# Optimization experiments

Hardware: AMD Instinct MI355X
Metric: run time of the kernel (lower is better)

Reference implementation:

```python
import jax, jax.numpy as jnp
import numpy as np
from jax import lax

_MS_SSIM_WEIGHTS = [0.0448, 0.2856, 0.3001, 0.2363, 0.1333]
LEVELS = 5
WINDOW_SIZE = 11
SIGMA = 1.5
DATA_RANGE = 2.0


def _gaussian_kernel(size, sigma, channels):
    x = jnp.arange(size, dtype=jnp.float32) - size // 2
    g = jnp.exp(-x ** 2 / (2.0 * sigma ** 2))
    g = g / g.sum()
    k2d = jnp.outer(g, g)  # [size, size]
    # depthwise kernel: [C, 1, size, size] (OIHW with feature_group_count=C)
    return jnp.broadcast_to(k2d[None, None], (channels, 1, size, size))


def _depthwise_conv(x, kernel, pad):
    C = x.shape[1]
    return lax.conv_general_dilated(
        x, kernel,
        window_strides=(1, 1),
        padding=[(pad, pad), (pad, pad)],
        dimension_numbers=('NCHW', 'OIHW', 'NCHW'),
        feature_group_count=C)


def _avg_pool2(x):
    s = lax.reduce_window(x, 0.0, lax.add, (1, 1, 2, 2), (1, 1, 2, 2), 'VALID')
    return s * 0.25


def _ssim(x, y, window_size=WINDOW_SIZE, sigma=SIGMA, data_range=DATA_RANGE):
    K1, K2 = 0.01, 0.03
    C1 = (K1 * data_range) ** 2
    C2 = (K2 * data_range) ** 2
    kernel = _gaussian_kernel(window_size, sigma, x.shape[1])
    pad = window_size // 2
    mu1 = _depthwise_conv(x, kernel, pad)
    mu2 = _depthwise_conv(y, kernel, pad)
    mu1_sq = mu1 * mu1
    mu2_sq = mu2 * mu2
    mu1_mu2 = mu1 * mu2
    sig1_sq = _depthwise_conv(x * x, kernel, pad) - mu1_sq
    sig2_sq = _depthwise_conv(y * y, kernel, pad) - mu2_sq
    sig12 = _depthwise_conv(x * y, kernel, pad) - mu1_mu2
    num = (2.0 * mu1_mu2 + C1) * (2.0 * sig12 + C2)
    den = (mu1_sq + mu2_sq + C1) * (sig1_sq + sig2_sq + C2)
    ssim_map = num / (den + 1e-8)
    return ssim_map.mean()


def setup_inputs() -> dict:
    key = jax.random.key(0)
    k1, k2 = jax.random.split(key)
    pred = jax.random.normal(k1, (16, 3, 512, 512), dtype=jnp.float32)
    target = jax.random.normal(k2, (16, 3, 512, 512), dtype=jnp.float32)
    return {"pred": pred, "target": target}


def reference(pred, target):
    weights = jnp.asarray(_MS_SSIM_WEIGHTS[:LEVELS], dtype=jnp.float32)
    weights = weights / weights.sum()
    ms_ssim_val = jnp.zeros((), dtype=jnp.float32)
    x, y = pred, target
    for i in range(LEVELS):
        s = _ssim(x, y)
        ms_ssim_val = ms_ssim_val + weights[i] * s
        if i < LEVELS - 1:
            x = _avg_pool2(x)
            y = _avg_pool2(y)
    return 1.0 - ms_ssim_val
```

## Files before the change

kernel.cpp:

```cpp
#include <hip/hip_runtime.h>


#define TW 32
#define NTHR 128
#define NIMG 48
#define WIN 42
#define PQ  32
#define NSLOT 256
#define SSTRIDE 16

#define RS1 272
#define RS2 144
#define RS3 80
#define RS4 48
#define IS0 (512L*512)
#define IS1 (256L*272)
#define IS2 (128L*144)
#define IS3 (64L*80)
#define IS4 (32L*48)

typedef float v4f __attribute__((ext_vector_type(4)));

struct Pyr {
    float *x1, *y1, *x2, *y2, *x3, *y3, *x4, *y4;
};

__device__ __forceinline__ void h_load(
    const float* __restrict__ xi, const float* __restrict__ yi,
    const float* __restrict__ zpad, int gr, int gc0, int H, int W,
    bool fastp, int rowStride, float* xv, float* yv)
{
    const bool rok = ((unsigned)gr < (unsigned)H);
    if (fastp) {
        const float* px = rok ? (xi + (long)gr * rowStride + gc0) : zpad;
        const float* py = rok ? (yi + (long)gr * rowStride + gc0) : zpad;
#pragma unroll
        for (int v = 0; v < 6; ++v) {
            const float4 a = reinterpret_cast<const float4*>(px)[v];
            const float4 b = reinterpret_cast<const float4*>(py)[v];
            xv[4*v+0]=a.x; xv[4*v+1]=a.y; xv[4*v+2]=a.z; xv[4*v+3]=a.w;
            yv[4*v+0]=b.x; yv[4*v+1]=b.y; yv[4*v+2]=b.z; yv[4*v+3]=b.w;
        }
    } else {
        const float* xrow = xi + (long)gr * rowStride;
        const float* yrow = yi + (long)gr * rowStride;
#pragma unroll
        for (int k = 3; k < 21; ++k) {
            const int gc = gc0 + k;
            const bool ok = rok && ((unsigned)gc < (unsigned)W);
            xv[k] = ok ? xrow[gc] : 0.0f;
            yv[k] = ok ? yrow[gc] : 0.0f;
        }
    }
}

__device__ __forceinline__ void h_conv_write(
    const float* xv, const float* yv, v4f* smA, int slot, int cb,
    const float* G)
{
    v4f s[8];
#pragma unroll
    for (int j = 0; j < 8; ++j) s[j] = {0.f, 0.f, 0.f, 0.f};
#pragma unroll
    for (int m = 0; m < 18; ++m) {
        const float a = xv[m+3], b = yv[m+3];
        v4f w; w.x = a; w.y = b; w.z = a*a + b*b; w.w = a*b;
#pragma unroll
        for (int j = 0; j < 8; ++j) {
            if (j <= m && m - j <= 10) {
                s[j] += w * G[m - j];
            }
        }
    }
    const int u = slot & 31;
#pragma unroll
    for (int j = 0; j < 8; ++j)
        smA[slot * PQ + ((cb + j) ^ u)] = s[j];
}

__device__ __forceinline__ float v_phase(
    const v4f* smA, int vb, int c, int rr0, int R0, int C0, int H, int W,
    const float* G)
{
    const float C1 = 4.0e-4f;
    const float C2 = 3.6e-3f;
    v4f acc[8];
#pragma unroll
    for (int i = 0; i < 8; ++i) acc[i] = {0.f, 0.f, 0.f, 0.f};
    int sl = vb;
#pragma unroll
    for (int k = 0; k < 18; ++k) {
        const v4f h = smA[sl * PQ + (c ^ (sl & 31))];
#pragma unroll
        for (int i = 0; i < 8; ++i) {
            if (i <= k && k - i <= 10) {
                acc[i] += h * G[k - i];
            }
        }
        sl = (sl + 1 == WIN) ? 0 : sl + 1;
    }
    float local = 0.f;
    const int gc = C0 + c;
#pragma unroll
    for (int i = 0; i < 8; ++i) {
        const int gr2 = R0 + rr0 + i;
        if (gr2 < H && gc < W) {
            const float mu1 = acc[i].x, mu2 = acc[i].y;
            const float mu1s = mu1*mu1, mu2s = mu2*mu2, m12 = mu1*mu2;
            const float ssum = acc[i].z - mu1s - mu2s;
            const float s12  = acc[i].w - m12;
            const float num = (2.f * m12 + C1) * (2.f * s12 + C2);
            const float den = (mu1s + mu2s + C1) * (ssum + C2);
            local += num * __builtin_amdgcn_rcpf(den + 1e-8f);
        }
    }
    return local;
}

__device__ __forceinline__ void pool_tree(
    const float* __restrict__ xi, const float* __restrict__ yi,
    int t, int R0, int C0, int z, const Pyr& p, int bx)
{
    const int r = t >> 3, c2 = t & 7;
    const int gr = R0 + 4 * r;
    const int gc = C0 + 4 * c2;

    float4 ax[4], ay[4];
#pragma unroll
    for (int rr = 0; rr < 4; ++rr) {
        ax[rr] = *reinterpret_cast<const float4*>(xi + (long)(gr+rr)*512 + gc);
        ay[rr] = *reinterpret_cast<const float4*>(yi + (long)(gr+rr)*512 + gc);
    }
    float qx[2][2], qy[2][2];
#pragma unroll
    for (int i = 0; i < 2; ++i) {
        qx[i][0] = 0.25f*(ax[2*i].x+ax[2*i].y+ax[2*i+1].x+ax[2*i+1].y);
        qx[i][1] = 0.25f*(ax[2*i].z+ax[2*i].w+ax[2*i+1].z+ax[2*i+1].w);
        qy[i][0] = 0.25f*(ay[2*i].x+ay[2*i].y+ay[2*i+1].x+ay[2*i+1].y);
        qy[i][1] = 0.25f*(ay[2*i].z+ay[2*i].w+ay[2*i+1].z+ay[2*i+1].w);
    }
    float* x1p = p.x1 + z*IS1;  float* y1p = p.y1 + z*IS1;
    float* x2p = p.x2 + z*IS2;  float* y2p = p.y2 + z*IS2;
    float* x3p = p.x3 + z*IS3;  float* y3p = p.y3 + z*IS3;
    float* x4p = p.x4 + z*IS4;  float* y4p = p.y4 + z*IS4;

    const int r1 = (R0 >> 1) + 2*r, c1 = (C0 >> 1) + 2*c2;
#pragma unroll
    for (int i = 0; i < 2; ++i) {
        *reinterpret_cast<float2*>(x1p + (long)(r1+i)*RS1 + c1) =
            make_float2(qx[i][0], qx[i][1]);
        *reinterpret_cast<float2*>(y1p + (long)(r1+i)*RS1 + c1) =
            make_float2(qy[i][0], qy[i][1]);
    }
    const float v2x = 0.25f*(qx[0][0]+qx[0][1]+qx[1][0]+qx[1][1]);
    const float v2y = 0.25f*(qy[0][0]+qy[0][1]+qy[1][0]+qy[1][1]);
    x2p[(long)((R0>>2)+r)*RS2 + (C0>>2)+c2] = v2x;
    y2p[(long)((R0>>2)+r)*RS2 + (C0>>2)+c2] = v2y;
    const float v3x = 0.25f*(v2x + __shfl_down(v2x,1,64)
                           + __shfl_down(v2x,8,64) + __shfl_down(v2x,9,64));
    const float v3y = 0.25f*(v2y + __shfl_down(v2y,1,64)
                           + __shfl_down(v2y,8,64) + __shfl_down(v2y,9,64));
    if (!(r & 1) && !(c2 & 1)) {
        x3p[(long)((R0>>3)+(r>>1))*RS3 + (C0>>3)+(c2>>1)] = v3x;
        y3p[(long)((R0>>3)+(r>>1))*RS3 + (C0>>3)+(c2>>1)] = v3y;
    }
    const float v4x = 0.25f*(v3x + __shfl_down(v3x,2,64)
                           + __shfl_down(v3x,16,64) + __shfl_down(v3x,18,64));
    const float v4y = 0.25f*(v3y + __shfl_down(v3y,2,64)
                           + __shfl_down(v3y,16,64) + __shfl_down(v3y,18,64));
    if (!(r & 3) && !(c2 & 3)) {
        x4p[(long)((R0>>4)+(r>>2))*RS4 + (C0>>4)+(c2>>2)] = v4x;
        y4p[(long)((R0>>4)+(r>>2))*RS4 + (C0>>4)+(c2>>2)] = v4y;
    }
    if (bx == 0) {
#pragma unroll
        for (int i = 0; i < 2; ++i) {
            x1p[(long)(r1+i)*RS1 + (c2-8)] = 0.f;
            y1p[(long)(r1+i)*RS1 + (c2-8)] = 0.f;
        }
        x2p[(long)((R0>>2)+r)*RS2 + (c2-8)] = 0.f;
        y2p[(long)((R0>>2)+r)*RS2 + (c2-8)] = 0.f;
        if (r < 4) { x3p[(long)((R0>>3)+r)*RS3 + (c2-8)] = 0.f;
                     y3p[(long)((R0>>3)+r)*RS3 + (c2-8)] = 0.f; }
        if (r < 2) { x4p[(long)((R0>>4)+r)*RS4 + (c2-8)] = 0.f;
                     y4p[(long)((R0>>4)+r)*RS4 + (c2-8)] = 0.f; }
    }
    if (bx == 15) {
#pragma unroll
        for (int i = 0; i < 2; ++i) {
            x1p[(long)(r1+i)*RS1 + 256 + c2] = 0.f;
            y1p[(long)(r1+i)*RS1 + 256 + c2] = 0.f;
        }
        x2p[(long)((R0>>2)+r)*RS2 + 128 + c2] = 0.f;
        y2p[(long)((R0>>2)+r)*RS2 + 128 + c2] = 0.f;
        if (r < 4) { x3p[(long)((R0>>3)+r)*RS3 + 64 + c2] = 0.f;
                     y3p[(long)((R0>>3)+r)*RS3 + 64 + c2] = 0.f; }
        if (r < 2) { x4p[(long)((R0>>4)+r)*RS4 + 32 + c2] = 0.f;
                     y4p[(long)((R0>>4)+r)*RS4 + 32 + c2] = 0.f; }
    }
}

__global__ __launch_bounds__(NTHR, 2) void ssim_l0_kernel(
    const float* __restrict__ x, const float* __restrict__ y,
    Pyr p, const float* __restrict__ zpad, float* __restrict__ slots)
{
    const float G[11] = {
        0.00102839f, 0.00759877f, 0.03600077f, 0.10936069f, 0.21300539f,
        0.26601173f, 0.21300539f, 0.10936069f, 0.03600077f, 0.00759877f,
        0.00102839f};

    __shared__ __align__(16) v4f smA[WIN * PQ];

    const int t    = threadIdx.x;
    const int bid  = blockIdx.x;
    const int tile = (bid & 7) * 384 + (bid >> 3);
    const int bx   = tile & 15;
    const int by   = (tile >> 4) & 3;
    const int z    = tile >> 6;
    const int C0   = bx * TW;
    const int S0   = by * 128;
    const float* xi = x + (long)z * IS0;
    const float* yi = y + (long)z * IS0;
    const bool fastp = (C0 >= 8) && (C0 + TW + 8 <= 512);

    for (int s = t; s < WIN * 4; s += NTHR) {
        const int r = s % WIN, q = s / WIN;
        float pxv[24], pyv[24];
        h_load(xi, yi, zpad, S0 + r - 5, C0 + (q << 3) - 8, 512, 512, fastp,
               512, pxv, pyv);
        h_conv_write(pxv, pyv, smA, r, q << 3, G);
    }
    __syncthreads();

    const int c    = t & 31;
    const int rr0  = (t >> 5) * 8;
    const int hr   = t & 31, hq = t >> 5;
    const int hgc0 = C0 + (hq << 3) - 8;
    int wslot = hr, vb = rr0;
    float local = 0.f;

    for (int tt = 0; tt < 3; ++tt) {
        const int R0 = S0 + 32 * tt;
        float xv[24], yv[24];
        h_load(xi, yi, zpad, R0 + 37 + hr, hgc0, 512, 512, fastp, 512, xv, yv);
        local += v_phase(smA, vb, c, rr0, R0, C0, 512, 512, G);
        if (t < 64) pool_tree(xi, yi, t, R0, C0, z, p, bx);
        __syncthreads();
        h_conv_write(xv, yv, smA, wslot, hq << 3, G);
        __syncthreads();
        wslot += 32; if (wslot >= WIN) wslot -= WIN;
        vb    += 32; if (vb    >= WIN) vb    -= WIN;
    }
    {
        const int R0 = S0 + 96;
        local += v_phase(smA, vb, c, rr0, R0, C0, 512, 512, G);
        if (t < 64) pool_tree(xi, yi, t, R0, C0, z, p, bx);
    }

#pragma unroll
    for (int off = 32; off > 0; off >>= 1) local += __shfl_down(local, off, 64);
    if ((t & 63) == 0) {
        const int slot = ((tile << 1) | (t >> 6)) & (NSLOT - 1);
        atomicAdd(slots + slot * SSTRIDE, local);
    }
}

__global__ __launch_bounds__(NTHR, 2) void ssim_lvls_kernel(
    Pyr p, const float* __restrict__ zpad, float* __restrict__ slots)
{
    const float G[11] = {
        0.00102839f, 0.00759877f, 0.03600077f, 0.10936069f, 0.21300539f,
        0.26601173f, 0.21300539f, 0.10936069f, 0.03600077f, 0.00759877f,
        0.00102839f};

    __shared__ __align__(16) v4f smA[WIN * PQ];

    const int t    = threadIdx.x;
    const int bid  = blockIdx.x;
    const int tile = (bid % 8) * 318 + (bid / 8);

    const float* xi; const float* yi;
    int rowStride, H, C0, S0, nsub, lvl, rem;
    if (tile < 1536) {
        rem = tile; lvl = 1; nsub = 2;
        const int bx = rem & 7, by = (rem >> 3) & 3, z = rem >> 5;
        xi = p.x1 + (long)z * IS1; yi = p.y1 + (long)z * IS1;
        rowStride = RS1; H = 256; C0 = bx * TW; S0 = by * 64;
    } else if (tile < 2304) {
        rem = tile - 1536; lvl = 2; nsub = 1;
        const int bx = rem & 3, by = (rem >> 2) & 3, z = rem >> 4;
        xi = p.x2 + (long)z * IS2; yi = p.y2 + (long)z * IS2;
        rowStride = RS2; H = 128; C0 = bx * TW; S0 = by * 32;
    } else if (tile < 2496) {
        rem = tile - 2304; lvl = 3; nsub = 1;
        const int bx = rem & 1, by = (rem >> 1) & 1, z = rem >> 2;
        xi = p.x3 + (long)z * IS3; yi = p.y3 + (long)z * IS3;
        rowStride = RS3; H = 64; C0 = bx * TW; S0 = by * 32;
    } else {
        rem = tile - 2496; lvl = 4; nsub = 1;
        const int z = rem;
        xi = p.x4 + (long)z * IS4; yi = p.y4 + (long)z * IS4;
        rowStride = RS4; H = 32; C0 = 0; S0 = 0;
    }

    for (int s = t; s < WIN * 4; s += NTHR) {
        const int r = s % WIN, q = s / WIN;
        float pxv[24], pyv[24];
        h_load(xi, yi, zpad, S0 + r - 5, C0 + (q << 3) - 8, H, H, true,
               rowStride, pxv, pyv);
        h_conv_write(pxv, pyv, smA, r, q << 3, G);
    }
    __syncthreads();

    const int c    = t & 31;
    const int rr0  = (t >> 5) * 8;
    const int hr   = t & 31, hq = t >> 5;
    int wslot = hr, vb = rr0;
    float local = 0.f;

    for (int tt = 0; tt < nsub - 1; ++tt) {
        const int R0 = S0 + 32 * tt;
        float xv[24], yv[24];
        h_load(xi, yi, zpad, R0 + 37 + hr, C0 + (hq << 3) - 8, H, H, true,
               rowStride, xv, yv);
        local += v_phase(smA, vb, c, rr0, R0, C0, H, H, G);
        __syncthreads();
        h_conv_write(xv, yv, smA, wslot, hq << 3, G);
        __syncthreads();
        wslot += 32; if (wslot >= WIN) wslot -= WIN;
        vb    += 32; if (vb    >= WIN) vb    -= WIN;
    }
    local += v_phase(smA, vb, c, rr0, S0 + 32 * (nsub - 1), C0, H, H, G);

#pragma unroll
    for (int off = 32; off > 0; off >>= 1) local += __shfl_down(local, off, 64);
    if ((t & 63) == 0) {
        const int slot = ((rem << 1) | (t >> 6)) & (NSLOT - 1);
        atomicAdd(slots + ((long)lvl * NSLOT + slot) * SSTRIDE, local);
    }
}

__global__ void finalize_kernel(const float* __restrict__ slots,
                                float* __restrict__ out)
{
    const int t = threadIdx.x;
    const float w[5] = {0.0448f, 0.2856f, 0.3001f, 0.2363f, 0.1333f};
    const float wsum = w[0] + w[1] + w[2] + w[3] + w[4];
    float acc = 0.f;
#pragma unroll
    for (int lvl = 0; lvl < 5; ++lvl) {
        const int d = 512 >> lvl;
        const float cnt = (float)NIMG * (float)d * (float)d;
        acc += (w[lvl] / wsum) / cnt * slots[(lvl * NSLOT + t) * SSTRIDE];
    }
#pragma unroll
    for (int off = 32; off > 0; off >>= 1) acc += __shfl_down(acc, off, 64);
    __shared__ float pp[4];
    if ((t & 63) == 0) pp[t >> 6] = acc;
    __syncthreads();
    if (t == 0) out[0] = 1.0f - (pp[0] + pp[1] + pp[2] + pp[3]);
}

extern "C" void kernel_launch(void* const* d_in, const int* in_sizes, int n_in,
                              void* d_out, int out_size, void* d_ws, size_t ws_size,
                              hipStream_t stream)
{
    const float* pred = (const float*)d_in[0];
    const float* targ = (const float*)d_in[1];
    float* out = (float*)d_out;
    float* ws  = (float*)d_ws;

    float* slots = ws;
    float* zpad  = slots + 5 * NSLOT * SSTRIDE;

    Pyr p;
    p.x1 = zpad + 640 + 8;
    p.y1 = p.x1 + NIMG * IS1;
    p.x2 = p.y1 + NIMG * IS1 - 8 + 8;
    p.x2 = p.y1 + NIMG * IS1;
    {
        float* b = zpad + 640;
        p.x1 = b + 8;                 b += NIMG * IS1;
        p.y1 = b + 8;                 b += NIMG * IS1;
        p.x2 = b + 8;                 b += NIMG * IS2;
        p.y2 = b + 8;                 b += NIMG * IS2;
        p.x3 = b + 8;                 b += NIMG * IS3;
        p.y3 = b + 8;                 b += NIMG * IS3;
        p.x4 = b + 8;                 b += NIMG * IS4;
        p.y4 = b + 8;
    }

    hipMemsetAsync(ws, 0, (size_t)(5 * NSLOT * SSTRIDE + 640) * sizeof(float),
                   stream);

    ssim_l0_kernel<<<dim3(3072), NTHR, 0, stream>>>(pred, targ, p, zpad, slots);
    ssim_lvls_kernel<<<dim3(2544), NTHR, 0, stream>>>(p, zpad, slots);

    finalize_kernel<<<1, 256, 0, stream>>>(slots, out);
}
```

Baseline: 233.5 us.

## Use taller column strips per block and split pooling work across both waves

The level-0 kernel now handles 256-row strips per block instead of 128, so the 10-row vertical halo is recomputed half as often. Pyramid pooling is split so each wave handles one image (x or y). Its global loads are issued before the vertical phase and the results are written after the barrier, which is meant to hide load latency. The lower-level kernel now gives each block a full column strip with more sub-iterations and fewer blocks, cutting halo recomputation. The trade-off is fewer blocks overall, which risks lower occupancy and poorer load balance across CUs on a large GPU, and more register pressure from the prefetched pool data.

```diff
diff --git a/kernel.cpp b/kernel.cpp
--- a/kernel.cpp
+++ b/kernel.cpp
@@ -117,86 +117,51 @@
     return local;
 }
 
-__device__ __forceinline__ void pool_tree(
-    const float* __restrict__ xi, const float* __restrict__ yi,
-    int t, int R0, int C0, int z, const Pyr& p, int bx)
-{
-    const int r = t >> 3, c2 = t & 7;
-    const int gr = R0 + 4 * r;
-    const int gc = C0 + 4 * c2;
-
-    float4 ax[4], ay[4];
-#pragma unroll
-    for (int rr = 0; rr < 4; ++rr) {
-        ax[rr] = *reinterpret_cast<const float4*>(xi + (long)(gr+rr)*512 + gc);
-        ay[rr] = *reinterpret_cast<const float4*>(yi + (long)(gr+rr)*512 + gc);
-    }
-    float qx[2][2], qy[2][2];
-#pragma unroll
-    for (int i = 0; i < 2; ++i) {
-        qx[i][0] = 0.25f*(ax[2*i].x+ax[2*i].y+ax[2*i+1].x+ax[2*i+1].y);
-        qx[i][1] = 0.25f*(ax[2*i].z+ax[2*i].w+ax[2*i+1].z+ax[2*i+1].w);
-        qy[i][0] = 0.25f*(ay[2*i].x+ay[2*i].y+ay[2*i+1].x+ay[2*i+1].y);
-        qy[i][1] = 0.25f*(ay[2*i].z+ay[2*i].w+ay[2*i+1].z+ay[2*i+1].w);
-    }
-    float* x1p = p.x1 + z*IS1;  float* y1p = p.y1 + z*IS1;
-    float* x2p = p.x2 + z*IS2;  float* y2p = p.y2 + z*IS2;
-    float* x3p = p.x3 + z*IS3;  float* y3p = p.y3 + z*IS3;
-    float* x4p = p.x4 + z*IS4;  float* y4p = p.y4 + z*IS4;
-
+__device__ __forceinline__ void pool_load(
+    const float* __restrict__ pi, int lane, int R0, int C0, float4* a)
+{
+    const int r = lane >> 3, c2 = lane & 7;
+    const float* s = pi + (long)(R0 + 4*r) * 512 + (C0 + 4*c2);
+#pragma unroll
+    for (int rr = 0; rr < 4; ++rr)
+        a[rr] = *reinterpret_cast<const float4*>(s + (long)rr * 512);
+}
+
+__device__ __forceinline__ void pool_finish(
+    const float4* a, int lane, int R0, int C0, int bx,
+    float* p1, float* p2, float* p3, float* p4)
+{
+    const int r = lane >> 3, c2 = lane & 7;
+    const float q00 = 0.25f*(a[0].x+a[0].y+a[1].x+a[1].y);
+    const float q01 = 0.25f*(a[0].z+a[0].w+a[1].z+a[1].w);
+    const float q10 = 0.25f*(a[2].x+a[2].y+a[3].x+a[3].y);
+    const float q11 = 0.25f*(a[2].z+a[2].w+a[3].z+a[3].w);
     const int r1 = (R0 >> 1) + 2*r, c1 = (C0 >> 1) + 2*c2;
-#pragma unroll
-    for (int i = 0; i < 2; ++i) {
-        *reinterpret_cast<float2*>(x1p + (long)(r1+i)*RS1 + c1) =
-            make_float2(qx[i][0], qx[i][1]);
-        *reinterpret_cast<float2*>(y1p + (long)(r1+i)*RS1 + c1) =
-            make_float2(qy[i][0], qy[i][1]);
-    }
-    const float v2x = 0.25f*(qx[0][0]+qx[0][1]+qx[1][0]+qx[1][1]);
-    const float v2y = 0.25f*(qy[0][0]+qy[0][1]+qy[1][0]+qy[1][1]);
-    x2p[(long)((R0>>2)+r)*RS2 + (C0>>2)+c2] = v2x;
-    y2p[(long)((R0>>2)+r)*RS2 + (C0>>2)+c2] = v2y;
-    const float v3x = 0.25f*(v2x + __shfl_down(v2x,1,64)
-                           + __shfl_down(v2x,8,64) + __shfl_down(v2x,9,64));
-    const float v3y = 0.25f*(v2y + __shfl_down(v2y,1,64)
-                           + __shfl_down(v2y,8,64) + __shfl_down(v2y,9,64));
-    if (!(r & 1) && !(c2 & 1)) {
-        x3p[(long)((R0>>3)+(r>>1))*RS3 + (C0>>3)+(c2>>1)] = v3x;
-        y3p[(long)((R0>>3)+(r>>1))*RS3 + (C0>>3)+(c2>>1)] = v3y;
-    }
-    const float v4x = 0.25f*(v3x + __shfl_down(v3x,2,64)
-                           + __shfl_down(v3x,16,64) + __shfl_down(v3x,18,64));
-    const float v4y = 0.25f*(v3y + __shfl_down(v3y,2,64)
-                           + __shfl_down(v3y,16,64) + __shfl_down(v3y,18,64));
-    if (!(r & 3) && !(c2 & 3)) {
-        x4p[(long)((R0>>4)+(r>>2))*RS4 + (C0>>4)+(c2>>2)] = v4x;
-        y4p[(long)((R0>>4)+(r>>2))*RS4 + (C0>>4)+(c2>>2)] = v4y;
-    }
+    *reinterpret_cast<float2*>(p1 + (long)r1*RS1 + c1) = make_float2(q00, q01);
+    *reinterpret_cast<float2*>(p1 + (long)(r1+1)*RS1 + c1) = make_float2(q10, q11);
+    const float v2 = 0.25f*(q00+q01+q10+q11);
+    p2[(long)((R0>>2)+r)*RS2 + (C0>>2)+c2] = v2;
+    const float v3 = 0.25f*(v2 + __shfl_down(v2,1,64)
+                          + __shfl_down(v2,8,64) + __shfl_down(v2,9,64));
+    if (!(r & 1) && !(c2 & 1))
+        p3[(long)((R0>>3)+(r>>1))*RS3 + (C0>>3)+(c2>>1)] = v3;
+    const float v4 = 0.25f*(v3 + __shfl_down(v3,2,64)
+                          + __shfl_down(v3,16,64) + __shfl_down(v3,18,64));
+    if (!(r & 3) && !(c2 & 3))
+        p4[(long)((R0>>4)+(r>>2))*RS4 + (C0>>4)+(c2>>2)] = v4;
     if (bx == 0) {
-#pragma unroll
-        for (int i = 0; i < 2; ++i) {
-            x1p[(long)(r1+i)*RS1 + (c2-8)] = 0.f;
-            y1p[(long)(r1+i)*RS1 + (c2-8)] = 0.f;
-        }
-        x2p[(long)((R0>>2)+r)*RS2 + (c2-8)] = 0.f;
-        y2p[(long)((R0>>2)+r)*RS2 + (c2-8)] = 0.f;
-        if (r < 4) { x3p[(long)((R0>>3)+r)*RS3 + (c2-8)] = 0.f;
-                     y3p[(long)((R0>>3)+r)*RS3 + (c2-8)] = 0.f; }
-        if (r < 2) { x4p[(long)((R0>>4)+r)*RS4 + (c2-8)] = 0.f;
-                     y4p[(long)((R0>>4)+r)*RS4 + (c2-8)] = 0.f; }
+        p1[(long)r1*RS1 + (c2-8)] = 0.f;
+        p1[(long)(r1+1)*RS1 + (c2-8)] = 0.f;
+        p2[(long)((R0>>2)+r)*RS2 + (c2-8)] = 0.f;
+        if (r < 4) p3[(long)((R0>>3)+r)*RS3 + (c2-8)] = 0.f;
+        if (r < 2) p4[(long)((R0>>4)+r)*RS4 + (c2-8)] = 0.f;
     }
     if (bx == 15) {
-#pragma unroll
-        for (int i = 0; i < 2; ++i) {
-            x1p[(long)(r1+i)*RS1 + 256 + c2] = 0.f;
-            y1p[(long)(r1+i)*RS1 + 256 + c2] = 0.f;
-        }
-        x2p[(long)((R0>>2)+r)*RS2 + 128 + c2] = 0.f;
-        y2p[(long)((R0>>2)+r)*RS2 + 128 + c2] = 0.f;
-        if (r < 4) { x3p[(long)((R0>>3)+r)*RS3 + 64 + c2] = 0.f;
-                     y3p[(long)((R0>>3)+r)*RS3 + 64 + c2] = 0.f; }
-        if (r < 2) { x4p[(long)((R0>>4)+r)*RS4 + 32 + c2] = 0.f;
-                     y4p[(long)((R0>>4)+r)*RS4 + 32 + c2] = 0.f; }
+        p1[(long)r1*RS1 + 256 + c2] = 0.f;
+        p1[(long)(r1+1)*RS1 + 256 + c2] = 0.f;
+        p2[(long)((R0>>2)+r)*RS2 + 128 + c2] = 0.f;
+        if (r < 4) p3[(long)((R0>>3)+r)*RS3 + 64 + c2] = 0.f;
+        if (r < 2) p4[(long)((R0>>4)+r)*RS4 + 32 + c2] = 0.f;
     }
 }
 
@@ -213,15 +178,22 @@
 
     const int t    = threadIdx.x;
     const int bid  = blockIdx.x;
-    const int tile = (bid & 7) * 384 + (bid >> 3);
+    const int tile = (bid & 7) * 192 + (bid >> 3);
     const int bx   = tile & 15;
-    const int by   = (tile >> 4) & 3;
-    const int z    = tile >> 6;
+    const int by   = (tile >> 4) & 1;
+    const int z    = tile >> 5;
     const int C0   = bx * TW;
-    const int S0   = by * 128;
+    const int S0   = by * 256;
     const float* xi = x + (long)z * IS0;
     const float* yi = y + (long)z * IS0;
     const bool fastp = (C0 >= 8) && (C0 + TW + 8 <= 512);
+
+    const int lane = t & 63;
+    const float* pimg = (t < 64) ? xi : yi;
+    float* q1 = ((t < 64) ? p.x1 : p.y1) + (long)z * IS1;
+    float* q2 = ((t < 64) ? p.x2 : p.y2) + (long)z * IS2;
+    float* q3 = ((t < 64) ? p.x3 : p.y3) + (long)z * IS3;
+    float* q4 = ((t < 64) ? p.x4 : p.y4) + (long)z * IS4;
 
     for (int s = t; s < WIN * 4; s += NTHR) {
         const int r = s % WIN, q = s / WIN;
@@ -239,22 +211,27 @@
     int wslot = hr, vb = rr0;
     float local = 0.f;
 
-    for (int tt = 0; tt < 3; ++tt) {
+#pragma unroll 1
+    for (int tt = 0; tt < 7; ++tt) {
         const int R0 = S0 + 32 * tt;
         float xv[24], yv[24];
         h_load(xi, yi, zpad, R0 + 37 + hr, hgc0, 512, 512, fastp, 512, xv, yv);
+        float4 pa[4];
+        pool_load(pimg, lane, R0, C0, pa);
         local += v_phase(smA, vb, c, rr0, R0, C0, 512, 512, G);
-        if (t < 64) pool_tree(xi, yi, t, R0, C0, z, p, bx);
         __syncthreads();
         h_conv_write(xv, yv, smA, wslot, hq << 3, G);
+        pool_finish(pa, lane, R0, C0, bx, q1, q2, q3, q4);
         __syncthreads();
         wslot += 32; if (wslot >= WIN) wslot -= WIN;
         vb    += 32; if (vb    >= WIN) vb    -= WIN;
     }
     {
-        const int R0 = S0 + 96;
+        const int R0 = S0 + 224;
+        float4 pa[4];
+        pool_load(pimg, lane, R0, C0, pa);
         local += v_phase(smA, vb, c, rr0, R0, C0, 512, 512, G);
-        if (t < 64) pool_tree(xi, yi, t, R0, C0, z, p, bx);
+        pool_finish(pa, lane, R0, C0, bx, q1, q2, q3, q4);
     }
 
 #pragma unroll
@@ -276,37 +253,36 @@
     __shared__ __align__(16) v4f smA[WIN * PQ];
 
     const int t    = threadIdx.x;
-    const int bid  = blockIdx.x;
-    const int tile = (bid % 8) * 318 + (bid / 8);
+    const int tile = blockIdx.x;
 
     const float* xi; const float* yi;
-    int rowStride, H, C0, S0, nsub, lvl, rem;
-    if (tile < 1536) {
-        rem = tile; lvl = 1; nsub = 2;
-        const int bx = rem & 7, by = (rem >> 3) & 3, z = rem >> 5;
+    int rowStride, H, C0, nsub, lvl, rem;
+    if (tile < 384) {
+        rem = tile; lvl = 1; nsub = 8;
+        const int bx = rem & 7, z = rem >> 3;
         xi = p.x1 + (long)z * IS1; yi = p.y1 + (long)z * IS1;
-        rowStride = RS1; H = 256; C0 = bx * TW; S0 = by * 64;
-    } else if (tile < 2304) {
-        rem = tile - 1536; lvl = 2; nsub = 1;
-        const int bx = rem & 3, by = (rem >> 2) & 3, z = rem >> 4;
+        rowStride = RS1; H = 256; C0 = bx * TW;
+    } else if (tile < 576) {
+        rem = tile - 384; lvl = 2; nsub = 4;
+        const int bx = rem & 3, z = rem >> 2;
         xi = p.x2 + (long)z * IS2; yi = p.y2 + (long)z * IS2;
-        rowStride = RS2; H = 128; C0 = bx * TW; S0 = by * 32;
-    } else if (tile < 2496) {
-        rem = tile - 2304; lvl = 3; nsub = 1;
-        const int bx = rem & 1, by = (rem >> 1) & 1, z = rem >> 2;
+        rowStride = RS2; H = 128; C0 = bx * TW;
+    } else if (tile < 672) {
+        rem = tile - 576; lvl = 3; nsub = 2;
+        const int bx = rem & 1, z = rem >> 1;
         xi = p.x3 + (long)z * IS3; yi = p.y3 + (long)z * IS3;
-        rowStride = RS3; H = 64; C0 = bx * TW; S0 = by * 32;
+        rowStride = RS3; H = 64; C0 = bx * TW;
     } else {
-        rem = tile - 2496; lvl = 4; nsub = 1;
+        rem = tile - 672; lvl = 4; nsub = 1;
         const int z = rem;
         xi = p.x4 + (long)z * IS4; yi = p.y4 + (long)z * IS4;
-        rowStride = RS4; H = 32; C0 = 0; S0 = 0;
+        rowStride = RS4; H = 32; C0 = 0;
     }
 
     for (int s = t; s < WIN * 4; s += NTHR) {
         const int r = s % WIN, q = s / WIN;
         float pxv[24], pyv[24];
-        h_load(xi, yi, zpad, S0 + r - 5, C0 + (q << 3) - 8, H, H, true,
+        h_load(xi, yi, zpad, r - 5, C0 + (q << 3) - 8, H, H, true,
                rowStride, pxv, pyv);
         h_conv_write(pxv, pyv, smA, r, q << 3, G);
     }
@@ -318,8 +294,9 @@
     int wslot = hr, vb = rr0;
     float local = 0.f;
 
-    for (int tt = 0; tt < nsub - 1; ++tt) {
-        const int R0 = S0 + 32 * tt;
+#pragma unroll 1
+    for (int tt = 0; tt + 1 < nsub; ++tt) {
+        const int R0 = 32 * tt;
         float xv[24], yv[24];
         h_load(xi, yi, zpad, R0 + 37 + hr, C0 + (hq << 3) - 8, H, H, true,
                rowStride, xv, yv);
@@ -330,7 +307,7 @@
         wslot += 32; if (wslot >= WIN) wslot -= WIN;
         vb    += 32; if (vb    >= WIN) vb    -= WIN;
     }
-    local += v_phase(smA, vb, c, rr0, S0 + 32 * (nsub - 1), C0, H, H, G);
+    local += v_phase(smA, vb, c, rr0, 32 * (nsub - 1), C0, H, H, G);
 
 #pragma unroll
     for (int off = 32; off > 0; off >>= 1) local += __shfl_down(local, off, 64);
@@ -374,10 +351,6 @@
     float* zpad  = slots + 5 * NSLOT * SSTRIDE;
 
     Pyr p;
-    p.x1 = zpad + 640 + 8;
-    p.y1 = p.x1 + NIMG * IS1;
-    p.x2 = p.y1 + NIMG * IS1 - 8 + 8;
-    p.x2 = p.y1 + NIMG * IS1;
     {
         float* b = zpad + 640;
         p.x1 = b + 8;                 b += NIMG * IS1;
@@ -393,8 +366,8 @@
     hipMemsetAsync(ws, 0, (size_t)(5 * NSLOT * SSTRIDE + 640) * sizeof(float),
                    stream);
 
-    ssim_l0_kernel<<<dim3(3072), NTHR, 0, stream>>>(pred, targ, p, zpad, slots);
-    ssim_lvls_kernel<<<dim3(2544), NTHR, 0, stream>>>(p, zpad, slots);
+    ssim_l0_kernel<<<dim3(1536), NTHR, 0, stream>>>(pred, targ, p, zpad, slots);
+    ssim_lvls_kernel<<<dim3(720), NTHR, 0, stream>>>(p, zpad, slots);
 
     finalize_kernel<<<1, 256, 0, stream>>>(slots, out);
 }
```

New measurement: 240.1 us. 1.03x slower.
